# Kernel tuning notes

Hardware: AMD Instinct MI355X
Metric: run time of the kernel (lower is better)

The kernel has to match this reference:

```python
import jax, jax.numpy as jnp
import numpy as np

# Stack of L SSA transformer blocks (SMVDR conv_trans stages with sr_ratio=2)
L, B, N, C = 4, 64, 196, 768          # layers, batch(=16 samples x 4 views), tokens, dim
CN = 960                               # c_new = int(C * 1.25)
HID = 3072                             # mlp hidden = 4*C
NH = 12                                # heads
HD, HDK = C // NH, CN // NH            # v head dim 64, q/k head dim 80
SR, HW = 2, 14                         # spatial reduction ratio, sqrt(N)


def _ln(x, g, b, eps):
    m = jnp.mean(x, axis=-1, keepdims=True)
    v = jnp.var(x, axis=-1, keepdims=True)
    return (x - m) * jax.lax.rsqrt(v + eps) * g + b


def setup_inputs() -> dict:
    key = jax.random.key(0)
    ks = jax.random.split(key, 12)
    s = jnp.float32(0.02)

    def rn(k, shape):
        return jax.random.normal(k, shape, jnp.float32) * s

    return {
        "x": jax.random.normal(ks[0], (B, N, C), jnp.float32),
        "q_w": rn(ks[1], (L, C, CN)),                 # q projection (no bias)
        "dw_w": rn(ks[2], (L, C, 1, SR, SR)),         # depthwise reduction conv (OIHW, groups=C)
        "dw_b": jnp.zeros((L, C), jnp.float32),
        "pw_w": rn(ks[3], (L, C, CN)),                # 1x1 conv C -> c_new
        "pw_b": jnp.zeros((L, CN), jnp.float32),
        "lnr_g": jnp.ones((L, CN), jnp.float32),      # norm_act LayerNorm (eps 1e-5)
        "lnr_b": jnp.zeros((L, CN), jnp.float32),
        "k_w": rn(ks[4], (L, CN, CN)),
        "v_w": rn(ks[5], (L, CN, C)),
        "proj_w": rn(ks[6], (L, C, C)),
        "proj_b": jnp.zeros((L, C), jnp.float32),
        "ln1_g": jnp.ones((L, C), jnp.float32),
        "ln1_b": jnp.zeros((L, C), jnp.float32),
        "ln2_g": jnp.ones((L, C), jnp.float32),
        "ln2_b": jnp.zeros((L, C), jnp.float32),
        "fc1_w": rn(ks[7], (L, C, HID)),
        "fc1_b": jnp.zeros((L, HID), jnp.float32),
        "fc2_w": rn(ks[8], (L, HID, C)),
        "fc2_b": jnp.zeros((L, C), jnp.float32),
    }


def reference(x, q_w, dw_w, dw_b, pw_w, pw_b, lnr_g, lnr_b, k_w, v_w,
              proj_w, proj_b, ln1_g, ln1_b, ln2_g, ln2_b,
              fc1_w, fc1_b, fc2_w, fc2_b):
    scale = 1.0 / jnp.sqrt(jnp.float32(HD) * 1.25)   # (head_dim * c_ratio) ** -0.5
    for l in range(L):
        # --- SSA attention branch ---
        y = _ln(x, ln1_g[l], ln1_b[l], 1e-6)
        img = y.transpose(0, 2, 1).reshape(B, C, HW, HW)
        # strided depthwise conv reduction (kernel=stride=sr_ratio, groups=C)
        r = jax.lax.conv_general_dilated(
            img, dw_w[l], window_strides=(SR, SR), padding='VALID',
            feature_group_count=C,
            dimension_numbers=('NCHW', 'OIHW', 'NCHW'))
        r = r + dw_b[l][None, :, None, None]
        r = jnp.einsum('bchw,cd->bhwd', r, pw_w[l]) + pw_b[l]   # 1x1 conv -> (B,7,7,CN)
        r = r.reshape(B, -1, CN)                                 # (B, M=49, CN)
        r = jax.nn.gelu(_ln(r, lnr_g[l], lnr_b[l], 1e-5), approximate=False)
        q = (y @ q_w[l]).reshape(B, N, NH, HDK).transpose(0, 2, 1, 3)   # (B,H,N,80)
        k = (r @ k_w[l]).reshape(B, -1, NH, HDK).transpose(0, 2, 1, 3)  # (B,H,M,80)
        v = (r @ v_w[l]).reshape(B, -1, NH, HD).transpose(0, 2, 1, 3)   # (B,H,M,64)
        attn = jax.nn.softmax(jnp.einsum('bhnd,bhmd->bhnm', q, k) * scale, axis=-1)
        o = jnp.einsum('bhnm,bhmd->bnhd', attn, v).reshape(B, N, C)
        x = x + o @ proj_w[l] + proj_b[l]
        # --- MLP branch ---
        z = _ln(x, ln2_g[l], ln2_b[l], 1e-6)
        h = jax.nn.gelu(z @ fc1_w[l] + fc1_b[l], approximate=False)
        x = x + h @ fc2_w[l] + fc2_b[l]
    return x
```

## Files before the change

### kernel.cpp

```cpp
#include <hip/hip_runtime.h>
#include <hip/hip_bf16.h>
#include <math.h>

#define L_LAYERS 4
#define BSZ 64
#define NTOK 196
#define CDIM 768
#define CNDIM 960
#define HIDDIM 3072
#define NHEAD 12
#define HD 64
#define HDK 80
#define MRED 49
#define ROWS (BSZ*NTOK)
#define RROWS (BSZ*MRED)
#define KVN 1728

typedef __bf16 bf16x8 __attribute__((ext_vector_type(8)));
typedef float f32x4 __attribute__((ext_vector_type(4)));
typedef unsigned short u16x4 __attribute__((ext_vector_type(4)));

static __device__ inline float bf2f(unsigned short u) {
    unsigned int x = ((unsigned int)u) << 16;
    return __builtin_bit_cast(float, x);
}
static __device__ inline unsigned short f2bf(float f) {
    return __builtin_bit_cast(unsigned short, __float2bfloat16(f));
}
static __device__ inline unsigned int pack2bf(float lo, float hi) {
    return (unsigned int)f2bf(lo) | ((unsigned int)f2bf(hi) << 16);
}
static __device__ inline float gelu_f(float x) {
    float t = x * (1.5957691216f + 0.0713548162f * x * x);
    return x * __builtin_amdgcn_rcpf(1.0f + __expf(-t));
}

#define GLLDS16(gsrc, ldst)                                                        \
    __builtin_amdgcn_global_load_lds(                                              \
        (const __attribute__((address_space(1))) unsigned int*)(const void*)(gsrc),\
        (__attribute__((address_space(3))) unsigned int*)(void*)(ldst), 16, 0, 0)

__global__ void transpose_bf16_kernel(const float* __restrict__ src,
                                      unsigned short* __restrict__ dst,
                                      int K, int N, size_t srcLS, size_t dstLS) {
    __shared__ float tile[32][33];
    const float* s = src + (size_t)blockIdx.z * srcLS;
    unsigned short* d = dst + (size_t)blockIdx.z * dstLS;
    int k0 = blockIdx.y * 32, n0 = blockIdx.x * 32;
#pragma unroll
    for (int i = 0; i < 4; i++) {
        int k = k0 + threadIdx.y + i * 8, n = n0 + threadIdx.x;
        if (k < K && n < N) tile[threadIdx.y + i * 8][threadIdx.x] = s[(size_t)k * N + n];
    }
    __syncthreads();
#pragma unroll
    for (int i = 0; i < 4; i++) {
        int n = n0 + threadIdx.y + i * 8, k = k0 + threadIdx.x;
        if (n < N && k < K) d[(size_t)n * K + k] = f2bf(tile[threadIdx.x][threadIdx.y + i * 8]);
    }
}

__global__ void ln_kernel(const float* __restrict__ x, const float* __restrict__ g,
                          const float* __restrict__ b, unsigned short* __restrict__ y,
                          int M, int C, float eps, int do_gelu) {
    int row = blockIdx.x * 4 + (threadIdx.x >> 6);
    int lane = threadIdx.x & 63;
    if (row >= M) return;
    const float* xr = x + (size_t)row * C;
    float s = 0.f, ss = 0.f;
    for (int c = lane; c < C; c += 64) { float v = xr[c]; s += v; ss += v * v; }
#pragma unroll
    for (int off = 32; off; off >>= 1) { s += __shfl_down(s, off); ss += __shfl_down(ss, off); }
    s = __shfl(s, 0); ss = __shfl(ss, 0);
    float mean = s / (float)C;
    float var = ss / (float)C - mean * mean;
    float rstd = rsqrtf(var + eps);
    unsigned short* yr = y + (size_t)row * C;
    for (int c = lane; c < C; c += 64) {
        float v = (xr[c] - mean) * rstd * g[c] + b[c];
        if (do_gelu) v = gelu_f(v);
        yr[c] = f2bf(v);
    }
}

__global__ void dwconv_kernel(const unsigned short* __restrict__ y,
                              const float* __restrict__ w,
                              const float* __restrict__ bias,
                              unsigned short* __restrict__ r0) {
    int bm = blockIdx.x;
    int b = bm / MRED, m = bm % MRED;
    int i = m / 7, j = m % 7;
    int r00 = b * NTOK + (2 * i) * 14 + 2 * j;
    for (int c = threadIdx.x; c < CDIM; c += 256) {
        float acc = bias[c];
        acc += bf2f(y[(size_t)(r00)      * CDIM + c]) * w[c * 4 + 0];
        acc += bf2f(y[(size_t)(r00 + 1)  * CDIM + c]) * w[c * 4 + 1];
        acc += bf2f(y[(size_t)(r00 + 14) * CDIM + c]) * w[c * 4 + 2];
        acc += bf2f(y[(size_t)(r00 + 15) * CDIM + c]) * w[c * 4 + 3];
        r0[(size_t)bm * CDIM + c] = f2bf(acc);
    }
}

template <int MODE>
__global__ __launch_bounds__(512, 4) void gemm128_kernel(
    const unsigned short* __restrict__ A,
    const unsigned short* __restrict__ Bt,
    const float* __restrict__ bias,
    float* __restrict__ outF,
    unsigned short* __restrict__ outB,
    int M, int N, int K, int NR, int NC) {
    extern __shared__ __align__(16) char sb[];

    int id = blockIdx.x;
    int gsize = 8 * NC;
    int g = id / gsize;
    int local = id - g * gsize;
    int rbase = g * 8;
    int Gg = NR - rbase; if (Gg > 8) Gg = 8;
    int col = local / Gg;
    int row = rbase + (local - col * Gg);
    int m0 = row * 128, n0 = col * 128;

    int tid = threadIdx.x;
    int w = tid >> 6, lane = tid & 63, quad = lane >> 4, l16 = lane & 15;
    int wm = w >> 2, wn = w & 3;

    int r = tid >> 3;
    int qc = (tid & 7) ^ (r & 7);
    const unsigned short* aS0 = A  + (size_t)(m0 + r) * K + qc * 8;
    const unsigned short* aS1 = A  + (size_t)(m0 + r + 64) * K + qc * 8;
    const unsigned short* bS0 = Bt + (size_t)(n0 + r) * K + qc * 8;
    const unsigned short* bS1 = Bt + (size_t)(n0 + r + 64) * K + qc * 8;

    int s7 = l16 & 7;
    int sq0 = ((0 + quad) ^ s7) * 16;
    int sq1 = ((4 + quad) ^ s7) * 16;
    int aBase = (wm * 64 + l16) * 128;
    int bBase = 16384 + (wn * 32 + l16) * 128;

    f32x4 zero4 = {0.f, 0.f, 0.f, 0.f};
    f32x4 acc[4][2];
#pragma unroll
    for (int mi = 0; mi < 4; mi++)
#pragma unroll
        for (int ni = 0; ni < 2; ni++) acc[mi][ni] = zero4;

    int NT = K >> 6;

#define STAGE64(slotptr, tt)                                     \
    do {                                                         \
        int ko_ = (tt) * 64;                                     \
        GLLDS16(aS0 + ko_, (slotptr) + w * 1024);                \
        GLLDS16(aS1 + ko_, (slotptr) + 8192  + w * 1024);        \
        GLLDS16(bS0 + ko_, (slotptr) + 16384 + w * 1024);        \
        GLLDS16(bS1 + ko_, (slotptr) + 24576 + w * 1024);        \
    } while (0)

    STAGE64(sb, 0);
    asm volatile("s_waitcnt vmcnt(0)" ::: "memory");
    __builtin_amdgcn_s_barrier();

    for (int t = 0; t < NT; ++t) {
        char* sc = sb + (size_t)(t & 1) * 32768;
        if (t + 1 < NT) {
            char* sp = sb + (size_t)((t + 1) & 1) * 32768;
            STAGE64(sp, t + 1);
        }
        bf16x8 af[4], bfr[2];
#pragma unroll
        for (int mi = 0; mi < 4; mi++)
            af[mi] = *(const bf16x8*)(sc + aBase + mi * 2048 + sq0);
#pragma unroll
        for (int ni = 0; ni < 2; ni++)
            bfr[ni] = *(const bf16x8*)(sc + bBase + ni * 2048 + sq0);
        __builtin_amdgcn_s_setprio(1);
#pragma unroll
        for (int mi = 0; mi < 4; mi++)
#pragma unroll
            for (int ni = 0; ni < 2; ni++)
                acc[mi][ni] = __builtin_amdgcn_mfma_f32_16x16x32_bf16(
                    af[mi], bfr[ni], acc[mi][ni], 0, 0, 0);
        __builtin_amdgcn_s_setprio(0);
#pragma unroll
        for (int mi = 0; mi < 4; mi++)
            af[mi] = *(const bf16x8*)(sc + aBase + mi * 2048 + sq1);
#pragma unroll
        for (int ni = 0; ni < 2; ni++)
            bfr[ni] = *(const bf16x8*)(sc + bBase + ni * 2048 + sq1);
        __builtin_amdgcn_s_setprio(1);
#pragma unroll
        for (int mi = 0; mi < 4; mi++)
#pragma unroll
            for (int ni = 0; ni < 2; ni++)
                acc[mi][ni] = __builtin_amdgcn_mfma_f32_16x16x32_bf16(
                    af[mi], bfr[ni], acc[mi][ni], 0, 0, 0);
        __builtin_amdgcn_s_setprio(0);
        asm volatile("s_waitcnt vmcnt(0)" ::: "memory");
        __builtin_amdgcn_s_barrier();
    }
#undef STAGE64

    __syncthreads();
    float* eld = (float*)(sb + w * 2048);
    int colbase = n0 + wn * 32;
#pragma unroll
    for (int mi = 0; mi < 4; mi++) {
#pragma unroll
        for (int ni = 0; ni < 2; ni++)
#pragma unroll
            for (int rr = 0; rr < 4; rr++)
                eld[(quad * 4 + rr) * 32 + ni * 16 + l16] = acc[mi][ni][rr];
        int rowb = m0 + wm * 64 + mi * 16;
#pragma unroll
        for (int p = 0; p < 2; p++) {
            int r2 = p * 8 + (lane >> 3);
            int c2 = (lane & 7) * 4;
            int gr = rowb + r2, gc = colbase + c2;
            if (gr < M && gc < N) {
                f32x4 v4 = *(f32x4*)(eld + r2 * 32 + c2);
                if (MODE == 0) {
                    u16x4 h;
#pragma unroll
                    for (int e = 0; e < 4; e++) h[e] = f2bf(v4[e]);
                    *(u16x4*)(outB + (size_t)gr * N + gc) = h;
                } else {
                    f32x4 b4 = *(const f32x4*)(bias + gc);
                    if (MODE == 1) {
                        *(f32x4*)(outF + (size_t)gr * N + gc) = v4 + b4;
                    } else if (MODE == 2) {
                        f32x4 o4 = *(f32x4*)(outF + (size_t)gr * N + gc);
                        *(f32x4*)(outF + (size_t)gr * N + gc) = o4 + v4 + b4;
                    } else {
                        u16x4 h;
#pragma unroll
                        for (int e = 0; e < 4; e++) h[e] = f2bf(gelu_f(v4[e] + b4[e]));
                        *(u16x4*)(outB + (size_t)gr * N + gc) = h;
                    }
                }
            }
        }
    }
}

__global__ __launch_bounds__(512, 4) void attn_kernel(
    const unsigned short* __restrict__ qb,
    const unsigned short* __restrict__ kv,
    unsigned short* __restrict__ ob) {
    __shared__ __align__(16) unsigned short Ks[64 * 96];
    __shared__ __align__(16) unsigned short V2[64 * 136];
    __shared__ __align__(16) unsigned short Os[8 * 16 * 72];

    int bh = blockIdx.x;
    int b = bh / NHEAD, h = bh % NHEAD;
    int tid = threadIdx.x;

    for (int idx = tid; idx < 49 * 8; idx += 512) {
        int m = idx >> 3, c = idx & 7;
        ((unsigned int*)Ks)[m * 48 + 40 + c] = 0u;
    }
    for (int idx = tid; idx < 49 * 10; idx += 512) {
        int m = idx / 10, c = idx % 10;
        bf16x8 v = *(const bf16x8*)(kv + (size_t)(b * MRED + m) * KVN + h * HDK + c * 8);
        *(bf16x8*)(Ks + m * 96 + c * 8) = v;
    }
    for (int idx = tid; idx < 64 * 128; idx += 512) {
        int d = idx >> 7, c = idx & 127;
        int s = c >> 5, q = (c >> 3) & 3, j = c & 7;
        int kt = s * 32 + ((j >> 2) << 4) + q * 4 + (j & 3);
        unsigned short val = 0;
        if (kt < MRED) val = kv[(size_t)(b * MRED + kt) * KVN + 960 + h * HD + d];
        V2[d * 136 + c] = val;
    }
    __syncthreads();

    int wv = tid >> 6, lane = tid & 63, quad = lane >> 4, l16 = lane & 15;
    unsigned short* Ow = Os + wv * 16 * 72;
    const float scale = 0.11180339887498949f;
    f32x4 zero4 = {0.f, 0.f, 0.f, 0.f};

#pragma unroll
    for (int gi = 0; gi < 2; ++gi) {
        int qg = wv + gi * 8;
        if (qg >= 13) break;
        const unsigned short* qrow =
            qb + (size_t)(b * NTOK + qg * 16 + l16) * CNDIM + h * HDK + quad * 8;
        bf16x8 bq0 = *(const bf16x8*)(qrow);
        bf16x8 bq1 = *(const bf16x8*)(qrow + 32);
        bf16x8 bq2 = *(const bf16x8*)(qrow + 64);

        f32x4 sf[4];
#pragma unroll
        for (int kf = 0; kf < 4; kf++) sf[kf] = zero4;
#pragma unroll
        for (int kf = 0; kf < 4; kf++) {
            const unsigned short* kr = Ks + (kf * 16 + l16) * 96 + quad * 8;
            sf[kf] = __builtin_amdgcn_mfma_f32_16x16x32_bf16(
                *(const bf16x8*)(kr), bq0, sf[kf], 0, 0, 0);
            sf[kf] = __builtin_amdgcn_mfma_f32_16x16x32_bf16(
                *(const bf16x8*)(kr + 32), bq1, sf[kf], 0, 0, 0);
            sf[kf] = __builtin_amdgcn_mfma_f32_16x16x32_bf16(
                *(const bf16x8*)(kr + 64), bq2, sf[kf], 0, 0, 0);
        }

        float p[4][4];
        float mx = -1e30f;
#pragma unroll
        for (int kf = 0; kf < 4; kf++)
#pragma unroll
            for (int r = 0; r < 4; r++) {
                float v = sf[kf][r] * scale;
                if (kf == 3) {
                    v = (r == 0 && quad == 0) ? v : -1e30f;
                }
                p[kf][r] = v;
                mx = fmaxf(mx, v);
            }
        mx = fmaxf(mx, __shfl_xor(mx, 16));
        mx = fmaxf(mx, __shfl_xor(mx, 32));
        float sum = 0.f;
#pragma unroll
        for (int kf = 0; kf < 4; kf++)
#pragma unroll
            for (int r = 0; r < 4; r++) {
                float e = __expf(p[kf][r] - mx);
                p[kf][r] = e;
                sum += e;
            }
        sum += __shfl_xor(sum, 16);
        sum += __shfl_xor(sum, 32);
        float inv = 1.0f / sum;
#pragma unroll
        for (int kf = 0; kf < 4; kf++)
#pragma unroll
            for (int r = 0; r < 4; r++) p[kf][r] *= inv;

        unsigned int W[4][2];
#pragma unroll
        for (int kf = 0; kf < 4; kf++) {
            W[kf][0] = pack2bf(p[kf][0], p[kf][1]);
            W[kf][1] = pack2bf(p[kf][2], p[kf][3]);
        }

        f32x4 oacc[4];
#pragma unroll
        for (int df = 0; df < 4; df++) oacc[df] = zero4;
#pragma unroll
        for (int s = 0; s < 2; s++) {
            union { unsigned int u[4]; bf16x8 v; } bb;
            bb.u[0] = W[2 * s][0];
            bb.u[1] = W[2 * s][1];
            bb.u[2] = W[2 * s + 1][0];
            bb.u[3] = W[2 * s + 1][1];
#pragma unroll
            for (int df = 0; df < 4; df++) {
                const unsigned short* vr = V2 + (df * 16 + l16) * 136 + s * 32 + quad * 8;
                oacc[df] = __builtin_amdgcn_mfma_f32_16x16x32_bf16(
                    *(const bf16x8*)(vr), bb.v, oacc[df], 0, 0, 0);
            }
        }

#pragma unroll
        for (int df = 0; df < 4; df++) {
#pragma unroll
            for (int wp = 0; wp < 2; wp++) {
                unsigned int pk = pack2bf(oacc[df][2 * wp], oacc[df][2 * wp + 1]);
                *(unsigned int*)(Ow + l16 * 72 + df * 16 + quad * 4 + 2 * wp) = pk;
            }
        }
        int q = lane >> 2, cch = lane & 3;
        int grow = qg * 16 + q;
        if (grow < NTOK) {
            unsigned short* dst = ob + (size_t)(b * NTOK + grow) * CDIM + h * HD + cch * 8;
            bf16x8 v0 = *(const bf16x8*)(Ow + q * 72 + cch * 8);
            bf16x8 v1 = *(const bf16x8*)(Ow + q * 72 + cch * 8 + 32);
            *(bf16x8*)(dst) = v0;
            *(bf16x8*)(dst + 32) = v1;
        }
    }
}


extern "C" void kernel_launch(void* const* d_in, const int* in_sizes, int n_in,
                              void* d_out, int out_size, void* d_ws, size_t ws_size,
                              hipStream_t stream) {
    (void)in_sizes; (void)n_in; (void)out_size; (void)ws_size;
    const float* x_in   = (const float*)d_in[0];
    const float* q_w    = (const float*)d_in[1];
    const float* dw_w   = (const float*)d_in[2];
    const float* dw_b   = (const float*)d_in[3];
    const float* pw_w   = (const float*)d_in[4];
    const float* pw_b   = (const float*)d_in[5];
    const float* lnr_g  = (const float*)d_in[6];
    const float* lnr_b  = (const float*)d_in[7];
    const float* k_w    = (const float*)d_in[8];
    const float* v_w    = (const float*)d_in[9];
    const float* proj_w = (const float*)d_in[10];
    const float* proj_b = (const float*)d_in[11];
    const float* ln1_g  = (const float*)d_in[12];
    const float* ln1_b  = (const float*)d_in[13];
    const float* ln2_g  = (const float*)d_in[14];
    const float* ln2_b  = (const float*)d_in[15];
    const float* fc1_w  = (const float*)d_in[16];
    const float* fc1_b  = (const float*)d_in[17];
    const float* fc2_w  = (const float*)d_in[18];
    const float* fc2_b  = (const float*)d_in[19];
    float* xout = (float*)d_out;
    char* ws = (char*)d_ws;

    static bool attr_done = false;
    if (!attr_done) {
        hipFuncSetAttribute(reinterpret_cast<const void*>(&gemm128_kernel<0>),
                            hipFuncAttributeMaxDynamicSharedMemorySize, 65536);
        hipFuncSetAttribute(reinterpret_cast<const void*>(&gemm128_kernel<1>),
                            hipFuncAttributeMaxDynamicSharedMemorySize, 65536);
        hipFuncSetAttribute(reinterpret_cast<const void*>(&gemm128_kernel<2>),
                            hipFuncAttributeMaxDynamicSharedMemorySize, 65536);
        hipFuncSetAttribute(reinterpret_cast<const void*>(&gemm128_kernel<3>),
                            hipFuncAttributeMaxDynamicSharedMemorySize, 65536);
        attr_done = true;
    }

    const size_t PL = 8601600;
    const size_t offQ = 0, offPW = 786432, offKV = 1572864,
                 offPJ = 3293184, offF1 = 3883008, offF2 = 6242304;
    unsigned short* W = (unsigned short*)ws;
    char* act = ws + PL * 2 * L_LAYERS;
    unsigned short* y_bf = (unsigned short*)act;
    char* blk = act + (size_t)ROWS * CDIM * 2;
    unsigned short* q_bf  = (unsigned short*)(blk);
    unsigned short* r0_bf = (unsigned short*)(blk + 24084480);
    float*          pw_f  = (float*)        (blk + 29196288);
    unsigned short* r_bf  = (unsigned short*)(blk + 41238528);
    unsigned short* kv_bf = (unsigned short*)(blk + 47628288);
    unsigned short* o_bf  = (unsigned short*)(blk + 58466304);
    unsigned short* h_bf  = (unsigned short*)(blk);
    unsigned short* z_bf  = y_bf;

    hipMemcpyAsync(xout, x_in, (size_t)ROWS * CDIM * sizeof(float),
                   hipMemcpyDeviceToDevice, stream);

    dim3 tb(32, 8);
    transpose_bf16_kernel<<<dim3(CNDIM / 32, CDIM / 32, L_LAYERS), tb, 0, stream>>>(
        q_w, W + offQ, CDIM, CNDIM, (size_t)CDIM * CNDIM, PL);
    transpose_bf16_kernel<<<dim3(CNDIM / 32, CDIM / 32, L_LAYERS), tb, 0, stream>>>(
        pw_w, W + offPW, CDIM, CNDIM, (size_t)CDIM * CNDIM, PL);
    transpose_bf16_kernel<<<dim3(CNDIM / 32, CNDIM / 32, L_LAYERS), tb, 0, stream>>>(
        k_w, W + offKV, CNDIM, CNDIM, (size_t)CNDIM * CNDIM, PL);
    transpose_bf16_kernel<<<dim3(CDIM / 32, CNDIM / 32, L_LAYERS), tb, 0, stream>>>(
        v_w, W + offKV + (size_t)CNDIM * CNDIM, CNDIM, CDIM, (size_t)CNDIM * CDIM, PL);
    transpose_bf16_kernel<<<dim3(CDIM / 32, CDIM / 32, L_LAYERS), tb, 0, stream>>>(
        proj_w, W + offPJ, CDIM, CDIM, (size_t)CDIM * CDIM, PL);
    transpose_bf16_kernel<<<dim3(HIDDIM / 32, CDIM / 32, L_LAYERS), tb, 0, stream>>>(
        fc1_w, W + offF1, CDIM, HIDDIM, (size_t)CDIM * HIDDIM, PL);
    transpose_bf16_kernel<<<dim3(CDIM / 32, HIDDIM / 32, L_LAYERS), tb, 0, stream>>>(
        fc2_w, W + offF2, HIDDIM, CDIM, (size_t)HIDDIM * CDIM, PL);

    for (int l = 0; l < L_LAYERS; l++) {
        const unsigned short* wl = W + (size_t)l * PL;
        ln_kernel<<<ROWS / 4, 256, 0, stream>>>(xout, ln1_g + l * CDIM, ln1_b + l * CDIM,
                                                y_bf, ROWS, CDIM, 1e-6f, 0);
        gemm128_kernel<0><<<98 * 8, 512, 65536, stream>>>(
            y_bf, wl + offQ, nullptr, nullptr, q_bf, ROWS, CNDIM, CDIM, 98, 8);
        dwconv_kernel<<<RROWS, 256, 0, stream>>>(y_bf, dw_w + (size_t)l * CDIM * 4,
                                                 dw_b + l * CDIM, r0_bf);
        gemm128_kernel<1><<<25 * 8, 512, 65536, stream>>>(
            r0_bf, wl + offPW, pw_b + l * CNDIM, pw_f, nullptr, RROWS, CNDIM, CDIM, 25, 8);
        ln_kernel<<<RROWS / 4, 256, 0, stream>>>(pw_f, lnr_g + l * CNDIM, lnr_b + l * CNDIM,
                                                 r_bf, RROWS, CNDIM, 1e-5f, 1);
        gemm128_kernel<0><<<25 * 14, 512, 65536, stream>>>(
            r_bf, wl + offKV, nullptr, nullptr, kv_bf, RROWS, KVN, CNDIM, 25, 14);
        attn_kernel<<<BSZ * NHEAD, 512, 0, stream>>>(q_bf, kv_bf, o_bf);
        gemm128_kernel<2><<<98 * 6, 512, 65536, stream>>>(
            o_bf, wl + offPJ, proj_b + l * CDIM, xout, nullptr, ROWS, CDIM, CDIM, 98, 6);
        ln_kernel<<<ROWS / 4, 256, 0, stream>>>(xout, ln2_g + l * CDIM, ln2_b + l * CDIM,
                                                z_bf, ROWS, CDIM, 1e-6f, 0);
        gemm128_kernel<3><<<98 * 24, 512, 65536, stream>>>(
            z_bf, wl + offF1, fc1_b + l * HIDDIM, nullptr, h_bf, ROWS, HIDDIM, CDIM, 98, 24);
        gemm128_kernel<2><<<98 * 6, 512, 65536, stream>>>(
            h_bf, wl + offF2, fc2_b + l * CDIM, xout, nullptr, ROWS, CDIM, HIDDIM, 98, 6);
    }
}
```

Baseline: 1.549 ms.

## Widen GEMM N-tile to 192 and add vectorized LayerNorm for C=768

Result: faster. 1.455 ms (-6.1%).

```diff
diff --git a/kernel.cpp b/kernel.cpp
--- a/kernel.cpp
+++ b/kernel.cpp
@@ -80,6 +80,40 @@
         float v = (xr[c] - mean) * rstd * g[c] + b[c];
         if (do_gelu) v = gelu_f(v);
         yr[c] = f2bf(v);
+    }
+}
+
+__global__ void ln768_kernel(const float* __restrict__ x, const float* __restrict__ g,
+                             const float* __restrict__ b, unsigned short* __restrict__ y,
+                             int M, float eps) {
+    int row = blockIdx.x * 4 + (threadIdx.x >> 6);
+    int lane = threadIdx.x & 63;
+    if (row >= M) return;
+    const float* xr = x + (size_t)row * 768;
+    f32x4 v[3];
+    float s = 0.f, ss = 0.f;
+#pragma unroll
+    for (int j = 0; j < 3; j++) {
+        v[j] = *(const f32x4*)(xr + j * 256 + lane * 4);
+#pragma unroll
+        for (int e = 0; e < 4; e++) { s += v[j][e]; ss += v[j][e] * v[j][e]; }
+    }
+#pragma unroll
+    for (int off = 32; off; off >>= 1) { s += __shfl_xor(s, off); ss += __shfl_xor(ss, off); }
+    const float invC = 1.0f / 768.0f;
+    float mean = s * invC;
+    float var = ss * invC - mean * mean;
+    float rstd = rsqrtf(var + eps);
+    unsigned short* yr = y + (size_t)row * 768;
+#pragma unroll
+    for (int j = 0; j < 3; j++) {
+        f32x4 gv = *(const f32x4*)(g + j * 256 + lane * 4);
+        f32x4 bv = *(const f32x4*)(b + j * 256 + lane * 4);
+        u16x4 h;
+#pragma unroll
+        for (int e = 0; e < 4; e++)
+            h[e] = f2bf((v[j][e] - mean) * rstd * gv[e] + bv[e]);
+        *(u16x4*)(yr + j * 256 + lane * 4) = h;
     }
 }
 
@@ -102,7 +136,7 @@
 }
 
 template <int MODE>
-__global__ __launch_bounds__(512, 4) void gemm128_kernel(
+__global__ __launch_bounds__(512, 4) void gemm192_kernel(
     const unsigned short* __restrict__ A,
     const unsigned short* __restrict__ Bt,
     const float* __restrict__ bias,
@@ -119,7 +153,7 @@
     int Gg = NR - rbase; if (Gg > 8) Gg = 8;
     int col = local / Gg;
     int row = rbase + (local - col * Gg);
-    int m0 = row * 128, n0 = col * 128;
+    int m0 = row * 128, n0 = col * 192;
 
     int tid = threadIdx.x;
     int w = tid >> 6, lane = tid & 63, quad = lane >> 4, l16 = lane & 15;
@@ -131,53 +165,55 @@
     const unsigned short* aS1 = A  + (size_t)(m0 + r + 64) * K + qc * 8;
     const unsigned short* bS0 = Bt + (size_t)(n0 + r) * K + qc * 8;
     const unsigned short* bS1 = Bt + (size_t)(n0 + r + 64) * K + qc * 8;
+    const unsigned short* bS2 = Bt + (size_t)(n0 + r + 128) * K + qc * 8;
 
     int s7 = l16 & 7;
     int sq0 = ((0 + quad) ^ s7) * 16;
     int sq1 = ((4 + quad) ^ s7) * 16;
     int aBase = (wm * 64 + l16) * 128;
-    int bBase = 16384 + (wn * 32 + l16) * 128;
+    int bBase = 16384 + (wn * 48 + l16) * 128;
 
     f32x4 zero4 = {0.f, 0.f, 0.f, 0.f};
-    f32x4 acc[4][2];
+    f32x4 acc[4][3];
 #pragma unroll
     for (int mi = 0; mi < 4; mi++)
 #pragma unroll
-        for (int ni = 0; ni < 2; ni++) acc[mi][ni] = zero4;
+        for (int ni = 0; ni < 3; ni++) acc[mi][ni] = zero4;
 
     int NT = K >> 6;
 
-#define STAGE64(slotptr, tt)                                     \
+#define STAGE192(slotptr, tt)                                    \
     do {                                                         \
         int ko_ = (tt) * 64;                                     \
         GLLDS16(aS0 + ko_, (slotptr) + w * 1024);                \
         GLLDS16(aS1 + ko_, (slotptr) + 8192  + w * 1024);        \
         GLLDS16(bS0 + ko_, (slotptr) + 16384 + w * 1024);        \
         GLLDS16(bS1 + ko_, (slotptr) + 24576 + w * 1024);        \
+        GLLDS16(bS2 + ko_, (slotptr) + 32768 + w * 1024);        \
     } while (0)
 
-    STAGE64(sb, 0);
+    STAGE192(sb, 0);
     asm volatile("s_waitcnt vmcnt(0)" ::: "memory");
     __builtin_amdgcn_s_barrier();
 
     for (int t = 0; t < NT; ++t) {
-        char* sc = sb + (size_t)(t & 1) * 32768;
+        char* sc = sb + (size_t)(t & 1) * 40960;
         if (t + 1 < NT) {
-            char* sp = sb + (size_t)((t + 1) & 1) * 32768;
-            STAGE64(sp, t + 1);
-        }
-        bf16x8 af[4], bfr[2];
+            char* sp = sb + (size_t)((t + 1) & 1) * 40960;
+            STAGE192(sp, t + 1);
+        }
+        bf16x8 af[4], bfr[3];
 #pragma unroll
         for (int mi = 0; mi < 4; mi++)
             af[mi] = *(const bf16x8*)(sc + aBase + mi * 2048 + sq0);
 #pragma unroll
-        for (int ni = 0; ni < 2; ni++)
+        for (int ni = 0; ni < 3; ni++)
             bfr[ni] = *(const bf16x8*)(sc + bBase + ni * 2048 + sq0);
         __builtin_amdgcn_s_setprio(1);
 #pragma unroll
         for (int mi = 0; mi < 4; mi++)
 #pragma unroll
-            for (int ni = 0; ni < 2; ni++)
+            for (int ni = 0; ni < 3; ni++)
                 acc[mi][ni] = __builtin_amdgcn_mfma_f32_16x16x32_bf16(
                     af[mi], bfr[ni], acc[mi][ni], 0, 0, 0);
         __builtin_amdgcn_s_setprio(0);
@@ -185,39 +221,41 @@
         for (int mi = 0; mi < 4; mi++)
             af[mi] = *(const bf16x8*)(sc + aBase + mi * 2048 + sq1);
 #pragma unroll
-        for (int ni = 0; ni < 2; ni++)
+        for (int ni = 0; ni < 3; ni++)
             bfr[ni] = *(const bf16x8*)(sc + bBase + ni * 2048 + sq1);
         __builtin_amdgcn_s_setprio(1);
 #pragma unroll
         for (int mi = 0; mi < 4; mi++)
 #pragma unroll
-            for (int ni = 0; ni < 2; ni++)
+            for (int ni = 0; ni < 3; ni++)
                 acc[mi][ni] = __builtin_amdgcn_mfma_f32_16x16x32_bf16(
                     af[mi], bfr[ni], acc[mi][ni], 0, 0, 0);
         __builtin_amdgcn_s_setprio(0);
         asm volatile("s_waitcnt vmcnt(0)" ::: "memory");
         __builtin_amdgcn_s_barrier();
     }
-#undef STAGE64
+#undef STAGE192
 
     __syncthreads();
-    float* eld = (float*)(sb + w * 2048);
-    int colbase = n0 + wn * 32;
+    float* eld = (float*)(sb + w * 3072);
+    int colbase = n0 + wn * 48;
 #pragma unroll
     for (int mi = 0; mi < 4; mi++) {
 #pragma unroll
-        for (int ni = 0; ni < 2; ni++)
+        for (int ni = 0; ni < 3; ni++)
 #pragma unroll
             for (int rr = 0; rr < 4; rr++)
-                eld[(quad * 4 + rr) * 32 + ni * 16 + l16] = acc[mi][ni][rr];
+                eld[(quad * 4 + rr) * 48 + ni * 16 + l16] = acc[mi][ni][rr];
         int rowb = m0 + wm * 64 + mi * 16;
 #pragma unroll
-        for (int p = 0; p < 2; p++) {
-            int r2 = p * 8 + (lane >> 3);
-            int c2 = (lane & 7) * 4;
+        for (int p = 0; p < 3; p++) {
+            int idx = p * 64 + lane;
+            int r2 = idx / 12;
+            int cg = idx - r2 * 12;
+            int c2 = cg * 4;
             int gr = rowb + r2, gc = colbase + c2;
             if (gr < M && gc < N) {
-                f32x4 v4 = *(f32x4*)(eld + r2 * 32 + c2);
+                f32x4 v4 = *(f32x4*)(eld + r2 * 48 + c2);
                 if (MODE == 0) {
                     u16x4 h;
 #pragma unroll
@@ -409,14 +447,14 @@
 
     static bool attr_done = false;
     if (!attr_done) {
-        hipFuncSetAttribute(reinterpret_cast<const void*>(&gemm128_kernel<0>),
-                            hipFuncAttributeMaxDynamicSharedMemorySize, 65536);
-        hipFuncSetAttribute(reinterpret_cast<const void*>(&gemm128_kernel<1>),
-                            hipFuncAttributeMaxDynamicSharedMemorySize, 65536);
-        hipFuncSetAttribute(reinterpret_cast<const void*>(&gemm128_kernel<2>),
-                            hipFuncAttributeMaxDynamicSharedMemorySize, 65536);
-        hipFuncSetAttribute(reinterpret_cast<const void*>(&gemm128_kernel<3>),
-                            hipFuncAttributeMaxDynamicSharedMemorySize, 65536);
+        hipFuncSetAttribute(reinterpret_cast<const void*>(&gemm192_kernel<0>),
+                            hipFuncAttributeMaxDynamicSharedMemorySize, 81920);
+        hipFuncSetAttribute(reinterpret_cast<const void*>(&gemm192_kernel<1>),
+                            hipFuncAttributeMaxDynamicSharedMemorySize, 81920);
+        hipFuncSetAttribute(reinterpret_cast<const void*>(&gemm192_kernel<2>),
+                            hipFuncAttributeMaxDynamicSharedMemorySize, 81920);
+        hipFuncSetAttribute(reinterpret_cast<const void*>(&gemm192_kernel<3>),
+                            hipFuncAttributeMaxDynamicSharedMemorySize, 81920);
         attr_done = true;
     }
 
@@ -457,26 +495,26 @@
 
     for (int l = 0; l < L_LAYERS; l++) {
         const unsigned short* wl = W + (size_t)l * PL;
-        ln_kernel<<<ROWS / 4, 256, 0, stream>>>(xout, ln1_g + l * CDIM, ln1_b + l * CDIM,
-                                                y_bf, ROWS, CDIM, 1e-6f, 0);
-        gemm128_kernel<0><<<98 * 8, 512, 65536, stream>>>(
-            y_bf, wl + offQ, nullptr, nullptr, q_bf, ROWS, CNDIM, CDIM, 98, 8);
+        ln768_kernel<<<ROWS / 4, 256, 0, stream>>>(xout, ln1_g + l * CDIM, ln1_b + l * CDIM,
+                                                   y_bf, ROWS, 1e-6f);
+        gemm192_kernel<0><<<98 * 5, 512, 81920, stream>>>(
+            y_bf, wl + offQ, nullptr, nullptr, q_bf, ROWS, CNDIM, CDIM, 98, 5);
         dwconv_kernel<<<RROWS, 256, 0, stream>>>(y_bf, dw_w + (size_t)l * CDIM * 4,
                                                  dw_b + l * CDIM, r0_bf);
-        gemm128_kernel<1><<<25 * 8, 512, 65536, stream>>>(
-            r0_bf, wl + offPW, pw_b + l * CNDIM, pw_f, nullptr, RROWS, CNDIM, CDIM, 25, 8);
+        gemm192_kernel<1><<<25 * 5, 512, 81920, stream>>>(
+            r0_bf, wl + offPW, pw_b + l * CNDIM, pw_f, nullptr, RROWS, CNDIM, CDIM, 25, 5);
         ln_kernel<<<RROWS / 4, 256, 0, stream>>>(pw_f, lnr_g + l * CNDIM, lnr_b + l * CNDIM,
                                                  r_bf, RROWS, CNDIM, 1e-5f, 1);
-        gemm128_kernel<0><<<25 * 14, 512, 65536, stream>>>(
-            r_bf, wl + offKV, nullptr, nullptr, kv_bf, RROWS, KVN, CNDIM, 25, 14);
+        gemm192_kernel<0><<<25 * 9, 512, 81920, stream>>>(
+            r_bf, wl + offKV, nullptr, nullptr, kv_bf, RROWS, KVN, CNDIM, 25, 9);
         attn_kernel<<<BSZ * NHEAD, 512, 0, stream>>>(q_bf, kv_bf, o_bf);
-        gemm128_kernel<2><<<98 * 6, 512, 65536, stream>>>(
-            o_bf, wl + offPJ, proj_b + l * CDIM, xout, nullptr, ROWS, CDIM, CDIM, 98, 6);
-        ln_kernel<<<ROWS / 4, 256, 0, stream>>>(xout, ln2_g + l * CDIM, ln2_b + l * CDIM,
-                                                z_bf, ROWS, CDIM, 1e-6f, 0);
-        gemm128_kernel<3><<<98 * 24, 512, 65536, stream>>>(
-            z_bf, wl + offF1, fc1_b + l * HIDDIM, nullptr, h_bf, ROWS, HIDDIM, CDIM, 98, 24);
-        gemm128_kernel<2><<<98 * 6, 512, 65536, stream>>>(
-            h_bf, wl + offF2, fc2_b + l * CDIM, xout, nullptr, ROWS, CDIM, HIDDIM, 98, 6);
-    }
-}
+        gemm192_kernel<2><<<98 * 4, 512, 81920, stream>>>(
+            o_bf, wl + offPJ, proj_b + l * CDIM, xout, nullptr, ROWS, CDIM, CDIM, 98, 4);
+        ln768_kernel<<<ROWS / 4, 256, 0, stream>>>(xout, ln2_g + l * CDIM, ln2_b + l * CDIM,
+                                                   z_bf, ROWS, 1e-6f);
+        gemm192_kernel<3><<<98 * 16, 512, 81920, stream>>>(
+            z_bf, wl + offF1, fc1_b + l * HIDDIM, nullptr, h_bf, ROWS, HIDDIM, CDIM, 98, 16);
+        gemm192_kernel<2><<<98 * 4, 512, 81920, stream>>>(
+            h_bf, wl + offF2, fc2_b + l * CDIM, xout, nullptr, ROWS, CDIM, HIDDIM, 98, 4);
+    }
+}
```
